# Performance work log

Measured on AMD Instinct MI355X. Metric: run time of the kernel, lower is better.

## Reference

```python
import jax, jax.numpy as jnp
import numpy as np
import math

D = 512
L = 1024
B = 2
N_SETS = 4
PLANES = 4
POS_PLANES = 16
TOTAL_PLANES = N_SETS * PLANES


def setup_inputs() -> dict:
    key = jax.random.key(0)
    ks = jax.random.split(key, 24)
    s = 0.02
    rn = lambda k, shp: jax.random.normal(k, shp, dtype=jnp.float32) * s
    inp = {
        "x": jax.random.normal(ks[0], (B, L, D), dtype=jnp.float32),
        # key encoder: Linear(D,D) -> GELU -> Linear(D,total_planes)
        "ke_w1": rn(ks[1], (D, D)), "ke_b1": jnp.zeros((D,), jnp.float32),
        "ke_w2": rn(ks[2], (D, TOTAL_PLANES)), "ke_b2": jnp.zeros((TOTAL_PLANES,), jnp.float32),
        # query encoder
        "qe_w1": rn(ks[3], (D, D)), "qe_b1": jnp.zeros((D,), jnp.float32),
        "qe_w2": rn(ks[4], (D, TOTAL_PLANES)), "qe_b2": jnp.zeros((TOTAL_PLANES,), jnp.float32),
        # to_value
        "v_w": rn(ks[5], (D, D)), "v_b": jnp.zeros((D,), jnp.float32),
        # to_out: LayerNorm(D) then Linear(D,D)
        "ln_g": jnp.ones((D,), jnp.float32), "ln_b": jnp.zeros((D,), jnp.float32),
        "out_w": rn(ks[6], (D, D)), "out_b": jnp.zeros((D,), jnp.float32),
        # set mixing weights, positional weight
        "set_weights": jnp.ones((N_SETS,), jnp.float32),
        "pos_weight": jnp.ones((1,), jnp.float32),
        # content_pos_gate: Linear(D, D//2) -> GELU -> Linear(D//2, 1) -> Sigmoid
        "gate_w1": rn(ks[7], (D, D // 2)), "gate_b1": jnp.zeros((D // 2,), jnp.float32),
        "gate_w2": rn(ks[8], (D // 2, 1)), "gate_b2": jnp.zeros((1,), jnp.float32),
        # positional frequencies (buffer)
        "pos_freqs": jnp.exp(jnp.arange(POS_PLANES, dtype=jnp.float32) * (-math.log(10000.0) / POS_PLANES)),
    }
    return inp


def reference(x, ke_w1, ke_b1, ke_w2, ke_b2, qe_w1, qe_b1, qe_w2, qe_b2,
              v_w, v_b, ln_g, ln_b, out_w, out_b, set_weights, pos_weight,
              gate_w1, gate_b1, gate_w2, gate_b2, pos_freqs):
    b, l, d = x.shape
    n_sets = set_weights.shape[0]
    total_planes = ke_w2.shape[1]
    planes = total_planes // n_sets

    gelu = lambda t: jax.nn.gelu(t, approximate=False)  # torch default GELU is exact

    key_phase = jnp.tanh(gelu(x @ ke_w1 + ke_b1) @ ke_w2 + ke_b2) * math.pi  # [B,L,P]
    query_phase = jnp.tanh(gelu(x @ qe_w1 + qe_b1) @ qe_w2 + qe_b2) * math.pi
    V = x @ v_w + v_b  # [B,L,D]

    kp = key_phase.reshape(b, l, n_sets, planes)
    qp = query_phase.reshape(b, l, n_sets, planes)
    w = jax.nn.softmax(set_weights)

    # complex phasor outer-product cumsum in real arithmetic:
    # bound = exp(i*kp) * V ; memory = cumsum_L(bound) ; retrieved = Re(memory * exp(-i*qp))
    Vb = V[:, :, None, None, :]                                   # [B,L,1,1,D]
    cum_re = jnp.cumsum(jnp.cos(kp)[..., None] * Vb, axis=1)      # [B,L,S,p,D]
    cum_im = jnp.cumsum(jnp.sin(kp)[..., None] * Vb, axis=1)
    retrieved = (cum_re * jnp.cos(qp)[..., None] + cum_im * jnp.sin(qp)[..., None]).sum(axis=3)  # [B,L,S,D]
    total_retrieved = jnp.einsum('blsd,s->bld', retrieved, w)

    # positional plane
    pos = jnp.arange(l, dtype=jnp.float32)[:, None]
    pos_phase = pos * pos_freqs * (2.0 * math.pi)                 # [L,PP]
    cp = jnp.cos(pos_phase)[None, :, :, None]                     # [1,L,PP,1]
    sp = jnp.sin(pos_phase)[None, :, :, None]
    Vp = V[:, :, None, :]                                          # [B,L,1,D]
    cumP_re = jnp.cumsum(cp * Vp, axis=1)                          # [B,L,PP,D]
    cumP_im = jnp.cumsum(sp * Vp, axis=1)
    retrieved_pos = (cumP_re * cp + cumP_im * sp).sum(axis=2)      # [B,L,D]

    gate = jax.nn.sigmoid(gelu(x @ gate_w1 + gate_b1) @ gate_w2 + gate_b2)  # [B,L,1]
    pos_contribution = jax.nn.sigmoid(pos_weight) * retrieved_pos
    total_retrieved = gate * total_retrieved + (1.0 - gate) * pos_contribution

    positions = jnp.arange(1, l + 1, dtype=jnp.float32)
    norm = jnp.sqrt(positions * planes)[None, :, None]
    h = total_retrieved / norm

    # to_out: LayerNorm then Linear
    mu = h.mean(axis=-1, keepdims=True)
    var = ((h - mu) ** 2).mean(axis=-1, keepdims=True)
    h_ln = (h - mu) / jnp.sqrt(var + 1e-5) * ln_g + ln_b
    return x + h_ln @ out_w + out_b
```

## Files before the change

kernel.cpp:

```cpp
#include <hip/hip_runtime.h>

typedef unsigned short u16;
typedef __attribute__((ext_vector_type(8))) __bf16 bf16x8;
typedef __attribute__((ext_vector_type(4))) float f32x4;

#define DI __device__ __forceinline__

DI u16 f2b(float f){ union{float f; unsigned u;} x; x.f = f; unsigned u = x.u;
  return (u16)((u + 0x7FFFu + ((u>>16)&1u)) >> 16); }

#define NCH 16
#define CLEN 64

__global__ __launch_bounds__(256) void k_prep(const float* __restrict__ x, u16* __restrict__ xb,
                            const float* w0, const float* w1, const float* w2, const float* w3, const float* w4,
                            u16* t0, u16* t1, u16* t2, u16* t3, u16* t4) {
  __shared__ u16 tile[32][33];
  int z = blockIdx.x;
  int t = threadIdx.x;
  if (z < 512) {
    int i = (z*256 + t)*8;
    float4 a = *(const float4*)(x+i);
    float4 b = *(const float4*)(x+i+4);
    unsigned o0 = (unsigned)f2b(a.x) | ((unsigned)f2b(a.y)<<16);
    unsigned o1 = (unsigned)f2b(a.z) | ((unsigned)f2b(a.w)<<16);
    unsigned o2 = (unsigned)f2b(b.x) | ((unsigned)f2b(b.y)<<16);
    unsigned o3 = (unsigned)f2b(b.z) | ((unsigned)f2b(b.w)<<16);
    *(uint4*)(xb+i) = make_uint4(o0,o1,o2,o3);
    return;
  }
  z -= 512;
  int which = z >> 8;
  int rem = z & 255;
  const float* src; u16* dst; int K, N;
  if (which==0){src=w0;dst=t0;K=512;N=512;}
  else if(which==1){src=w1;dst=t1;K=512;N=512;}
  else if(which==2){src=w2;dst=t2;K=512;N=512;}
  else if(which==3){src=w3;dst=t3;K=512;N=256;}
  else             {src=w4;dst=t4;K=512;N=512;}
  int n0 = (rem & 15)*32, k0 = (rem >> 4)*32;
  if (n0 >= N) return;
  int tx = t & 31, ty = t >> 5;
  #pragma unroll
  for (int r = 0; r < 4; r++) tile[ty + 8*r][tx] = f2b(src[(k0 + ty + 8*r)*N + n0 + tx]);
  __syncthreads();
  #pragma unroll
  for (int r = 0; r < 4; r++) dst[(n0 + ty + 8*r)*K + k0 + tx] = tile[tx][ty + 8*r];
}

#define GEMM64_LOOP(APTR, BPTR)                                                       \
  __shared__ short As[2][64][72];                                                     \
  __shared__ short Bs[2][64][72];                                                     \
  int t = threadIdx.x;                                                                \
  int lane = t & 63, wid = t >> 6;                                                    \
  int wm = (wid>>1)*32, wn = (wid&1)*32;                                              \
  int lr = lane & 15, ls = lane >> 4;                                                 \
  int srow = t >> 2, scol = (t & 3)*16;                                               \
  f32x4 acc[2][2];                                                                    \
  { f32x4 z_={0.f,0.f,0.f,0.f}; acc[0][0]=z_;acc[0][1]=z_;acc[1][0]=z_;acc[1][1]=z_; }\
  const u16* gA = (APTR) + (bm+srow)*512 + scol;                                      \
  const u16* gB = (BPTR) + (bn+srow)*512 + scol;                                      \
  bf16x8 rA0 = *(const bf16x8*)(gA);      bf16x8 rA1 = *(const bf16x8*)(gA+8);        \
// ... 10 lines not shown
    _Pragma("unroll")                                                                 \
    for (int ks = 0; ks < 2; ks++) {                                                  \
      _Pragma("unroll")                                                               \
      for (int mi = 0; mi < 2; mi++) {                                                \
        af_[mi][ks] = *(const bf16x8*)&As[cur][wm+mi*16+lr][ks*32+ls*8];              \
        bf_[mi][ks] = *(const bf16x8*)&Bs[cur][wn+mi*16+lr][ks*32+ls*8];              \
      }                                                                               \
    }                                                                                 \
    if (st < 7) {                                                                     \
      *(bf16x8*)&As[cur^1][srow][scol] = nA0; *(bf16x8*)&As[cur^1][srow][scol+8] = nA1; \
      *(bf16x8*)&Bs[cur^1][srow][scol] = nB0; *(bf16x8*)&Bs[cur^1][srow][scol+8] = nB1; \
    }                                                                                 \
    if (st < 6) {                                                                     \
      int kk = (st+2)*64;                                                             \
      nA0 = *(const bf16x8*)(gA+kk);    nA1 = *(const bf16x8*)(gA+kk+8);              \
      nB0 = *(const bf16x8*)(gB+kk);    nB1 = *(const bf16x8*)(gB+kk+8);              \
    }                                                                                 \
    _Pragma("unroll")                                                                 \
    for (int ks = 0; ks < 2; ks++)                                                    \
      _Pragma("unroll")                                                               \
      for (int mi = 0; mi < 2; mi++)                                                  \
        _Pragma("unroll")                                                             \
        for (int ni = 0; ni < 2; ni++)                                                \
          acc[mi][ni] = __builtin_amdgcn_mfma_f32_16x16x32_bf16(af_[mi][ks], bf_[ni][ks], acc[mi][ni], 0,0,0); \
    __syncthreads();                                                                  \
  }

__global__ __launch_bounds__(256) void k_gemm4(const u16* __restrict__ A, const u16* __restrict__ BTF,
                       const float* __restrict__ kb1, const float* __restrict__ qb1,
                       const float* __restrict__ vb,  const float* __restrict__ gbias1,
                       float* __restrict__ Hke, float* __restrict__ Hqe,
                       float* __restrict__ V,   float* __restrict__ Hg) {
  int bm = blockIdx.y*64, bn = blockIdx.x*64;
  GEMM64_LOOP(A, BTF)
  float* C; const float* bias; int nstr, nb; bool gel;
  if (bn < 512)       { C=Hke; bias=kb1;    nstr=512; nb=bn;      gel=true;  }
  else if (bn < 1024) { C=Hqe; bias=qb1;    nstr=512; nb=bn-512;  gel=true;  }
  else if (bn < 1536) { C=V;   bias=vb;     nstr=512; nb=bn-1024; gel=false; }
  else                { C=Hg;  bias=gbias1; nstr=256; nb=bn-1536; gel=true;  }
  #pragma unroll
  for (int mi = 0; mi < 2; mi++)
    #pragma unroll
    for (int ni = 0; ni < 2; ni++)
      #pragma unroll
      for (int r = 0; r < 4; r++) {
        int grow = bm + wm + mi*16 + ls*4 + r;
        int gcol = nb + wn + ni*16 + lr;
        float v = acc[mi][ni][r] + bias[gcol];
        if (gel) v = 0.5f*v*(1.0f + erff(v*0.70710678118654752f));
        C[grow*nstr + gcol] = v;
      }
}

__global__ __launch_bounds__(256) void k_gemm_out(const u16* __restrict__ A, const u16* __restrict__ BT,
                       const float* __restrict__ bias, const float* __restrict__ resid,
                       float* __restrict__ C) {
  int bm = blockIdx.y*64, bn = blockIdx.x*64;
  GEMM64_LOOP(A, BT)
  #pragma unroll
  for (int mi = 0; mi < 2; mi++)
    #pragma unroll
    for (int ni = 0; ni < 2; ni++)
      #pragma unroll
      for (int r = 0; r < 4; r++) {
        int grow = bm + wm + mi*16 + ls*4 + r;
        int gcol = bn + wn + ni*16 + lr;
        float v = acc[mi][ni][r] + bias[gcol] + resid[grow*512 + gcol];
        C[grow*512 + gcol] = v;
      }
}

__global__ __launch_bounds__(256) void k_phase(const float* __restrict__ Hke, const float* __restrict__ Hqe,
                        const float* __restrict__ Hg,
                        const float* __restrict__ kw2, const float* __restrict__ kb2,
                        const float* __restrict__ qw2, const float* __restrict__ qb2,
                        const float* __restrict__ gw2, const float* __restrict__ gb2,
                        const float* __restrict__ setw, const float* __restrict__ posw,
                        const float* __restrict__ freqs,
                        float* __restrict__ ub, float* __restrict__ ab) {
  int t = threadIdx.x;
  int wid = t >> 6, lane = t & 63;
  int r = blockIdx.x*4 + wid;
  int l = r & 1023;
  int p = lane & 15, s = lane >> 4;
  const float* hk = Hke + r*512 + s*128;
  const float* hq = Hqe + r*512 + s*128;
  float kps = 0.f, qps = 0.f;
  for (int i0 = 0; i0 < 128; i0 += 4) {
    float4 hkv = *(const float4*)(hk + i0);
    float4 hqv = *(const float4*)(hq + i0);
    int kb = (s*128 + i0)*16 + p;
    kps += hkv.x * kw2[kb];      qps += hqv.x * qw2[kb];
    kps += hkv.y * kw2[kb+16];   qps += hqv.y * qw2[kb+16];
    kps += hkv.z * kw2[kb+32];   qps += hqv.z * qw2[kb+32];
    kps += hkv.w * kw2[kb+48];   qps += hqv.w * qw2[kb+48];
  }
  kps += __shfl_xor(kps, 16); kps += __shfl_xor(kps, 32);
  qps += __shfl_xor(qps, 16); qps += __shfl_xor(qps, 32);
  const float PI = 3.14159265358979323846f;
  float kph = tanhf(kps + kb2[p]) * PI;
  float qph = tanhf(qps + qb2[p]) * PI;
  const float* hg = Hg + r*256;
  float4 hgv = *(const float4*)(hg + lane*4);
  float gp = hgv.x*gw2[lane*4] + hgv.y*gw2[lane*4+1]
           + hgv.z*gw2[lane*4+2] + hgv.w*gw2[lane*4+3];
  #pragma unroll
  for (int m = 1; m <= 32; m <<= 1) gp += __shfl_xor(gp, m);
  float gate = 1.f/(1.f + expf(-(gp + gb2[0])));
  float pph = (float)l * freqs[p] * 6.2831853071795864769f;
  float s0=setw[0], s1=setw[1], s2=setw[2], s3=setw[3];
  float mx = fmaxf(fmaxf(s0,s1), fmaxf(s2,s3));
  float e0=expf(s0-mx), e1=expf(s1-mx), e2=expf(s2-mx), e3=expf(s3-mx);
  float esum = e0+e1+e2+e3;
  int si = p >> 2;
  float wsel = (si==0? e0 : si==1? e1 : si==2? e2 : e3) / esum;
  float sigpw = 1.f/(1.f + expf(-posw[0]));
  float invnorm = rsqrtf((float)(l+1) * 4.0f);
  if (lane < 16) {
    float sk, ck, sq, cq, sp, cp;
    sincosf(kph, &sk, &ck);
    sincosf(qph, &sq, &cq);
    sincosf(pph, &sp, &cp);
    float* urow = ub + r*64;
    float* arow = ab + r*64;
    urow[p]      = ck;
    urow[16 + p] = sk;
    urow[32 + p] = cp;
    urow[48 + p] = sp;
    float ga = gate * wsel * invnorm;
    float pa = (1.f - gate) * sigpw * invnorm;
    arow[p]      = ga * cq;
    arow[16 + p] = ga * sq;
    arow[32 + p] = pa * cp;
    arow[48 + p] = pa * sp;
  }
}

__global__ __launch_bounds__(256) void k_scanA(const float* __restrict__ ub, const float* __restrict__ V,
                        float* __restrict__ P) {
  __shared__ float ul[CLEN][64];
  __shared__ float vl[CLEN][64];
  int t = threadIdx.x;
  int d0 = blockIdx.x*64; int c = blockIdx.y; int b = blockIdx.z;
  int srow = t >> 2, scol = (t & 3)*16;
  {
    const float* up = ub + (b*1024 + c*CLEN + srow)*64 + scol;
    *(float4*)&ul[srow][scol]    = *(const float4*)up;
    *(float4*)&ul[srow][scol+4]  = *(const float4*)(up+4);
    *(float4*)&ul[srow][scol+8]  = *(const float4*)(up+8);
    *(float4*)&ul[srow][scol+12] = *(const float4*)(up+12);
    const float* vp = V + (b*1024 + c*CLEN + srow)*512 + d0 + scol;
    *(float4*)&vl[srow][scol]    = *(const float4*)vp;
    *(float4*)&vl[srow][scol+4]  = *(const float4*)(vp+4);
    *(float4*)&vl[srow][scol+8]  = *(const float4*)(vp+8);
    *(float4*)&vl[srow][scol+12] = *(const float4*)(vp+12);
  }
  __syncthreads();
  int dd = t & 63, kg = t >> 6;
  float acc[16];
  #pragma unroll
  for (int i=0;i<16;i++) acc[i]=0.f;
  for (int tt = 0; tt < CLEN; tt++) {
    float vv = vl[tt][dd];
    #pragma unroll
    for (int i=0;i<16;i++) acc[i] += ul[tt][kg*16+i]*vv;
  }
  float* pp = P + (((b*NCH + c)*64) + kg*16)*512 + d0 + dd;
  #pragma unroll
  for (int i=0;i<16;i++) pp[i*512] = acc[i];
}

__global__ __launch_bounds__(256) void k_scanB(float* __restrict__ P) {
  int tid = blockIdx.x*256 + threadIdx.x;
  int b = tid >> 15;
  int k = (tid >> 9) & 63;
  int d = tid & 511;
  float run = 0.f;
  float* base = P + ((b*NCH)*64 + k)*512 + d;
  for (int c = 0; c < NCH; c++) {
    float v = base[c*64*512];
    base[c*64*512] = run;
    run += v;
  }
}

__global__ __launch_bounds__(256) void k_scanC(const float* __restrict__ ub, const float* __restrict__ ab,
                        const float* __restrict__ V, const float* __restrict__ P,
                        float* __restrict__ h) {
  __shared__ float ul[CLEN][64];
  __shared__ float al[CLEN][64];
  int t = threadIdx.x;
  int c = blockIdx.y; int b = blockIdx.z;
  int srow = t >> 2, scol = (t & 3)*16;
  {
    const float* up = ub + (b*1024 + c*CLEN + srow)*64 + scol;
    *(float4*)&ul[srow][scol]    = *(const float4*)up;
    *(float4*)&ul[srow][scol+4]  = *(const float4*)(up+4);
    *(float4*)&ul[srow][scol+8]  = *(const float4*)(up+8);
    *(float4*)&ul[srow][scol+12] = *(const float4*)(up+12);
    const float* ap = ab + (b*1024 + c*CLEN + srow)*64 + scol;
    *(float4*)&al[srow][scol]    = *(const float4*)ap;
    *(float4*)&al[srow][scol+4]  = *(const float4*)(ap+4);
    *(float4*)&al[srow][scol+8]  = *(const float4*)(ap+8);
    *(float4*)&al[srow][scol+12] = *(const float4*)(ap+12);
  }
  __syncthreads();
  int kg = t & 3;
  int di = t >> 2;
  int d = blockIdx.x*64 + di;
  float s[16];
  const float* pb = P + ((b*NCH + c)*64 + kg*16)*512 + d;
  #pragma unroll
  for (int k = 0; k < 16; k++) s[k] = pb[k*512];
  const float* vrow = V + (b*1024 + c*CLEN)*512 + d;
  float* hrow = h + (b*1024 + c*CLEN)*512 + d;
  const float4* ul4 = (const float4*)&ul[0][0];
  const float4* al4 = (const float4*)&al[0][0];
  for (int tt = 0; tt < CLEN; tt++) {
    float vv = vrow[tt*512];
    float4 u0 = ul4[tt*16 + kg*4 + 0];
    float4 u1 = ul4[tt*16 + kg*4 + 1];
    float4 u2 = ul4[tt*16 + kg*4 + 2];
    float4 u3 = ul4[tt*16 + kg*4 + 3];
    float4 a0 = al4[tt*16 + kg*4 + 0];
    float4 a1 = al4[tt*16 + kg*4 + 1];
    float4 a2 = al4[tt*16 + kg*4 + 2];
    float4 a3 = al4[tt*16 + kg*4 + 3];
    float h0=0.f, h1=0.f, h2=0.f, h3=0.f;
    s[0]  += u0.x*vv; h0 += a0.x*s[0];
    s[1]  += u0.y*vv; h1 += a0.y*s[1];
    s[2]  += u0.z*vv; h2 += a0.z*s[2];
    s[3]  += u0.w*vv; h3 += a0.w*s[3];
    s[4]  += u1.x*vv; h0 += a1.x*s[4];
    s[5]  += u1.y*vv; h1 += a1.y*s[5];
    s[6]  += u1.z*vv; h2 += a1.z*s[6];
    s[7]  += u1.w*vv; h3 += a1.w*s[7];
    s[8]  += u2.x*vv; h0 += a2.x*s[8];
    s[9]  += u2.y*vv; h1 += a2.y*s[9];
    s[10] += u2.z*vv; h2 += a2.z*s[10];
    s[11] += u2.w*vv; h3 += a2.w*s[11];
    s[12] += u3.x*vv; h0 += a3.x*s[12];
    s[13] += u3.y*vv; h1 += a3.y*s[13];
    s[14] += u3.z*vv; h2 += a3.z*s[14];
    s[15] += u3.w*vv; h3 += a3.w*s[15];
    float hp = (h0+h1)+(h2+h3);
    hp += __shfl_xor(hp, 1);
    hp += __shfl_xor(hp, 2);
    if (kg == 0) hrow[tt*512] = hp;
  }
}

__global__ __launch_bounds__(256) void k_ln(const float* __restrict__ h, const float* __restrict__ g,
                     const float* __restrict__ bta, u16* __restrict__ hln) {
  int t = threadIdx.x;
  int wid = t >> 6, lane = t & 63;
  int r = blockIdx.x*4 + wid;
  const float* hr = h + r*512;
  float4 v0 = *(const float4*)(hr + lane*8);
  float4 v1 = *(const float4*)(hr + lane*8 + 4);
  float vals[8] = {v0.x,v0.y,v0.z,v0.w,v1.x,v1.y,v1.z,v1.w};
  float sum = 0.f, sq = 0.f;
  #pragma unroll
  for (int i=0;i<8;i++){ sum += vals[i]; sq += vals[i]*vals[i]; }
  #pragma unroll
  for (int m = 1; m <= 32; m <<= 1){ sum += __shfl_xor(sum, m); sq += __shfl_xor(sq, m); }
  float mu = sum * (1.f/512.f);
  float var = sq * (1.f/512.f) - mu*mu;
  float rstd = rsqrtf(var + 1e-5f);
  unsigned o[4];
  #pragma unroll
  for (int i=0;i<4;i++){
    u16 lo = f2b((vals[2*i]  -mu)*rstd*g[lane*8+2*i]   + bta[lane*8+2*i]);
    u16 hi = f2b((vals[2*i+1]-mu)*rstd*g[lane*8+2*i+1] + bta[lane*8+2*i+1]);
    o[i] = (unsigned)lo | ((unsigned)hi << 16);
  }
  uint4 ov = make_uint4(o[0],o[1],o[2],o[3]);
  *(uint4*)(hln + r*512 + lane*8) = ov;
}

extern "C" void kernel_launch(void* const* d_in, const int* in_sizes, int n_in,
                              void* d_out, int out_size, void* d_ws, size_t ws_size,
                              hipStream_t stream) {
  const float* x       = (const float*)d_in[0];
  const float* ke_w1   = (const float*)d_in[1];
  const float* ke_b1   = (const float*)d_in[2];
  const float* ke_w2   = (const float*)d_in[3];
  const float* ke_b2   = (const float*)d_in[4];
  const float* qe_w1   = (const float*)d_in[5];
  const float* qe_b1   = (const float*)d_in[6];
  const float* qe_w2   = (const float*)d_in[7];
  const float* qe_b2   = (const float*)d_in[8];
  const float* v_w     = (const float*)d_in[9];
  const float* v_b     = (const float*)d_in[10];
  const float* ln_g    = (const float*)d_in[11];
  const float* ln_b    = (const float*)d_in[12];
  const float* out_w   = (const float*)d_in[13];
  const float* out_b   = (const float*)d_in[14];
  const float* setw    = (const float*)d_in[15];
  const float* posw    = (const float*)d_in[16];
  const float* gate_w1 = (const float*)d_in[17];
  const float* gate_b1 = (const float*)d_in[18];
  const float* gate_w2 = (const float*)d_in[19];
  const float* gate_b2 = (const float*)d_in[20];
  const float* freqs   = (const float*)d_in[21];
  float* out = (float*)d_out;

  char* ws = (char*)d_ws;
  u16*   xb  = (u16*)(ws + 0);
  u16*   BTF = (u16*)(ws + 2097152);
  u16*   oT  = (u16*)(ws + 3932160);
  float* Hke = (float*)(ws + 4456448);
  float* Hqe = (float*)(ws + 8650752);
  float* Hg  = (float*)(ws + 12845056);
  float* V   = (float*)(ws + 14942208);
  float* ubf = (float*)(ws + 19136512);
  float* abf = (float*)(ws + 19660800);
  float* P   = (float*)(ws + 20185088);
  float* h   = Hke;
  u16*   hln = (u16*)Hqe;

  u16* keT = BTF;
  u16* qeT = BTF + 512*512;
  u16* vT  = BTF + 1024*512;
  u16* gT  = BTF + 1536*512;

  k_prep<<<512 + 5*256, 256, 0, stream>>>(x, xb, ke_w1,qe_w1,v_w,gate_w1,out_w,
                                          keT,qeT,vT,gT,oT);
  k_gemm4<<<dim3(28,32),256,0,stream>>>(xb, BTF, ke_b1, qe_b1, v_b, gate_b1,
                                        Hke, Hqe, V, Hg);
  k_phase<<<512,256,0,stream>>>(Hke,Hqe,Hg, ke_w2,ke_b2, qe_w2,qe_b2,
                                gate_w2,gate_b2, setw,posw,freqs, ubf,abf);
  k_scanA<<<dim3(8,NCH,2),256,0,stream>>>(ubf, V, P);
  k_scanB<<<256,256,0,stream>>>(P);
  k_scanC<<<dim3(8,NCH,2),256,0,stream>>>(ubf, abf, V, P, h);
  k_ln<<<512,256,0,stream>>>(h, ln_g, ln_b, hln);
  k_gemm_out<<<dim3(8,32),256,0,stream>>>(hln, oT, out_b, x, out);
}
```

Before: 78.64 us.

## Fuse LayerNorm into output GEMM and scanB into scanA via last-block counter

Removes the standalone LayerNorm kernel: the output GEMM now computes per-row mean and rstd from fp32 h, then normalizes and converts to bf16 while staging A tiles into double-buffered LDS. Folds the cross-chunk prefix pass into scanA, where the last arriving block per (batch, d-tile) runs the carry scan, detected with an atomic counter that k_phase resets. This saves two launches and the hln round trip. The cost is that each GEMM block re-reads its 64 rows of h to get statistics, and the tail scan runs serially in only 16 blocks.

```diff
diff --git a/kernel.cpp b/kernel.cpp
--- a/kernel.cpp
+++ b/kernel.cpp
@@ -8,6 +8,12 @@
 
 DI u16 f2b(float f){ union{float f; unsigned u;} x; x.f = f; unsigned u = x.u;
   return (u16)((u + 0x7FFFu + ((u>>16)&1u)) >> 16); }
+
+DI uint2 ln4(float4 a, float4 g, float4 c, float mu, float rs) {
+  unsigned lo = (unsigned)f2b((a.x-mu)*rs*g.x+c.x) | ((unsigned)f2b((a.y-mu)*rs*g.y+c.y)<<16);
+  unsigned hi = (unsigned)f2b((a.z-mu)*rs*g.z+c.z) | ((unsigned)f2b((a.w-mu)*rs*g.w+c.w)<<16);
+  return make_uint2(lo,hi);
+}
 
 #define NCH 16
 #define CLEN 64
@@ -124,11 +130,104 @@
       }
 }
 
-__global__ __launch_bounds__(256) void k_gemm_out(const u16* __restrict__ A, const u16* __restrict__ BT,
+__global__ __launch_bounds__(256) void k_gemm_out_ln(
+                       const float* __restrict__ h,   const float* __restrict__ lng,
+                       const float* __restrict__ lnb, const u16* __restrict__ BT,
                        const float* __restrict__ bias, const float* __restrict__ resid,
                        float* __restrict__ C) {
+  __shared__ short As[2][64][72];
+  __shared__ short Bs[2][64][72];
+  __shared__ float mu_s[64], rs_s[64];
+  int t = threadIdx.x;
   int bm = blockIdx.y*64, bn = blockIdx.x*64;
-  GEMM64_LOOP(A, BT)
+  int lane = t & 63, wid = t >> 6;
+  int wm = (wid>>1)*32, wn = (wid&1)*32;
+  int lr = lane & 15, ls = lane >> 4;
+  int srow = t >> 2, scol = (t & 3)*16;
+  {
+    int rr = t >> 2, q = t & 3;
+    const float* hr = h + (bm + rr)*512 + q*128;
+    float sum = 0.f, sq = 0.f;
+    #pragma unroll
+    for (int i = 0; i < 128; i += 4) {
+      float4 v = *(const float4*)(hr + i);
+      sum += (v.x+v.y)+(v.z+v.w);
+      sq  += (v.x*v.x+v.y*v.y)+(v.z*v.z+v.w*v.w);
+    }
+    sum += __shfl_xor(sum,1); sum += __shfl_xor(sum,2);
+    sq  += __shfl_xor(sq,1);  sq  += __shfl_xor(sq,2);
+    if (q == 0) {
+      float m_ = sum * (1.f/512.f);
+      float var = sq * (1.f/512.f) - m_*m_;
+      mu_s[rr] = m_;
+      rs_s[rr] = rsqrtf(var + 1e-5f);
+    }
+  }
+  __syncthreads();
+  const float mu = mu_s[srow], rs = rs_s[srow];
+  f32x4 acc[2][2];
+  { f32x4 z_={0.f,0.f,0.f,0.f}; acc[0][0]=z_;acc[0][1]=z_;acc[1][0]=z_;acc[1][1]=z_; }
+  const float* gA = h + (bm+srow)*512 + scol;
+  const u16*  gB = BT + (bn+srow)*512 + scol;
+  float4 a0,a1,a2,a3, n0,n1,n2,n3;
+  bf16x8 rB0, rB1, nB0, nB1;
+  a0=*(const float4*)(gA);    a1=*(const float4*)(gA+4);
+  a2=*(const float4*)(gA+8);  a3=*(const float4*)(gA+12);
+  rB0=*(const bf16x8*)(gB);   rB1=*(const bf16x8*)(gB+8);
+  n0=*(const float4*)(gA+64); n1=*(const float4*)(gA+68);
+  n2=*(const float4*)(gA+72); n3=*(const float4*)(gA+76);
+  nB0=*(const bf16x8*)(gB+64); nB1=*(const bf16x8*)(gB+72);
+  {
+    float4 g0=*(const float4*)(lng+scol),   g1=*(const float4*)(lng+scol+4);
+    float4 g2=*(const float4*)(lng+scol+8), g3=*(const float4*)(lng+scol+12);
+    float4 c0=*(const float4*)(lnb+scol),   c1=*(const float4*)(lnb+scol+4);
+    float4 c2=*(const float4*)(lnb+scol+8), c3=*(const float4*)(lnb+scol+12);
+    uint2 p0=ln4(a0,g0,c0,mu,rs), p1=ln4(a1,g1,c1,mu,rs);
+    uint2 p2=ln4(a2,g2,c2,mu,rs), p3=ln4(a3,g3,c3,mu,rs);
+    *(uint4*)&As[0][srow][scol]   = make_uint4(p0.x,p0.y,p1.x,p1.y);
+    *(uint4*)&As[0][srow][scol+8] = make_uint4(p2.x,p2.y,p3.x,p3.y);
+    *(bf16x8*)&Bs[0][srow][scol] = rB0; *(bf16x8*)&Bs[0][srow][scol+8] = rB1;
+  }
+  __syncthreads();
+  #pragma unroll
+  for (int st = 0; st < 8; st++) {
+    int cur = st & 1;
+    bf16x8 af_[2][2], bf_[2][2];
+    #pragma unroll
+    for (int ks = 0; ks < 2; ks++) {
+      #pragma unroll
+      for (int mi = 0; mi < 2; mi++) {
+        af_[mi][ks] = *(const bf16x8*)&As[cur][wm+mi*16+lr][ks*32+ls*8];
+        bf_[mi][ks] = *(const bf16x8*)&Bs[cur][wn+mi*16+lr][ks*32+ls*8];
+      }
+    }
+    if (st < 7) {
+      int kc = (st+1)*64 + scol;
+      float4 g0=*(const float4*)(lng+kc),   g1=*(const float4*)(lng+kc+4);
+      float4 g2=*(const float4*)(lng+kc+8), g3=*(const float4*)(lng+kc+12);
+      float4 c0=*(const float4*)(lnb+kc),   c1=*(const float4*)(lnb+kc+4);
+      float4 c2=*(const float4*)(lnb+kc+8), c3=*(const float4*)(lnb+kc+12);
+      uint2 p0=ln4(n0,g0,c0,mu,rs), p1=ln4(n1,g1,c1,mu,rs);
+      uint2 p2=ln4(n2,g2,c2,mu,rs), p3=ln4(n3,g3,c3,mu,rs);
+      *(uint4*)&As[cur^1][srow][scol]   = make_uint4(p0.x,p0.y,p1.x,p1.y);
+      *(uint4*)&As[cur^1][srow][scol+8] = make_uint4(p2.x,p2.y,p3.x,p3.y);
+      *(bf16x8*)&Bs[cur^1][srow][scol] = nB0; *(bf16x8*)&Bs[cur^1][srow][scol+8] = nB1;
+    }
+    if (st < 6) {
+      int kk = (st+2)*64;
+      n0=*(const float4*)(gA+kk);    n1=*(const float4*)(gA+kk+4);
+      n2=*(const float4*)(gA+kk+8);  n3=*(const float4*)(gA+kk+12);
+      nB0=*(const bf16x8*)(gB+kk);   nB1=*(const bf16x8*)(gB+kk+8);
+    }
+    #pragma unroll
+    for (int ks = 0; ks < 2; ks++)
+      #pragma unroll
+      for (int mi = 0; mi < 2; mi++)
+        #pragma unroll
+        for (int ni = 0; ni < 2; ni++)
+          acc[mi][ni] = __builtin_amdgcn_mfma_f32_16x16x32_bf16(af_[mi][ks], bf_[ni][ks], acc[mi][ni], 0,0,0);
+    __syncthreads();
+  }
   #pragma unroll
   for (int mi = 0; mi < 2; mi++)
     #pragma unroll
@@ -149,8 +248,10 @@
                         const float* __restrict__ gw2, const float* __restrict__ gb2,
                         const float* __restrict__ setw, const float* __restrict__ posw,
                         const float* __restrict__ freqs,
-                        float* __restrict__ ub, float* __restrict__ ab) {
+                        float* __restrict__ ub, float* __restrict__ ab,
+                        int* __restrict__ counters) {
   int t = threadIdx.x;
+  if (blockIdx.x == 0 && t < 16) counters[t] = 0;
   int wid = t >> 6, lane = t & 63;
   int r = blockIdx.x*4 + wid;
   int l = r & 1023;
@@ -209,9 +310,10 @@
 }
 
 __global__ __launch_bounds__(256) void k_scanA(const float* __restrict__ ub, const float* __restrict__ V,
-                        float* __restrict__ P) {
+                        float* __restrict__ P, int* __restrict__ counters) {
   __shared__ float ul[CLEN][64];
   __shared__ float vl[CLEN][64];
+  __shared__ int lastf;
   int t = threadIdx.x;
   int d0 = blockIdx.x*64; int c = blockIdx.y; int b = blockIdx.z;
   int srow = t >> 2, scol = (t & 3)*16;
@@ -240,19 +342,26 @@
   float* pp = P + (((b*NCH + c)*64) + kg*16)*512 + d0 + dd;
   #pragma unroll
   for (int i=0;i<16;i++) pp[i*512] = acc[i];
-}
-
-__global__ __launch_bounds__(256) void k_scanB(float* __restrict__ P) {
-  int tid = blockIdx.x*256 + threadIdx.x;
-  int b = tid >> 15;
-  int k = (tid >> 9) & 63;
-  int d = tid & 511;
-  float run = 0.f;
-  float* base = P + ((b*NCH)*64 + k)*512 + d;
-  for (int c = 0; c < NCH; c++) {
-    float v = base[c*64*512];
-    base[c*64*512] = run;
-    run += v;
+  __threadfence();
+  if (t == 0) {
+    int old = atomicAdd(&counters[b*8 + blockIdx.x], 1);
+    lastf = (old == NCH-1) ? 1 : 0;
+  }
+  __syncthreads();
+  if (lastf) {
+    int d = d0 + (t & 63);
+    int kq0 = (t >> 6) * 16;
+    #pragma unroll 1
+    for (int kq = 0; kq < 16; kq++) {
+      float run = 0.f;
+      float* base = P + ((b*NCH)*64 + kq0 + kq)*512 + d;
+      #pragma unroll 1
+      for (int c2 = 0; c2 < NCH; c2++) {
+        float v = base[c2*64*512];
+        base[c2*64*512] = run;
+        run += v;
+      }
+    }
   }
 }
 
@@ -322,34 +431,6 @@
   }
 }
 
-__global__ __launch_bounds__(256) void k_ln(const float* __restrict__ h, const float* __restrict__ g,
-                     const float* __restrict__ bta, u16* __restrict__ hln) {
-  int t = threadIdx.x;
-  int wid = t >> 6, lane = t & 63;
-  int r = blockIdx.x*4 + wid;
-  const float* hr = h + r*512;
-  float4 v0 = *(const float4*)(hr + lane*8);
-  float4 v1 = *(const float4*)(hr + lane*8 + 4);
-  float vals[8] = {v0.x,v0.y,v0.z,v0.w,v1.x,v1.y,v1.z,v1.w};
-  float sum = 0.f, sq = 0.f;
-  #pragma unroll
-  for (int i=0;i<8;i++){ sum += vals[i]; sq += vals[i]*vals[i]; }
-  #pragma unroll
-  for (int m = 1; m <= 32; m <<= 1){ sum += __shfl_xor(sum, m); sq += __shfl_xor(sq, m); }
-  float mu = sum * (1.f/512.f);
-  float var = sq * (1.f/512.f) - mu*mu;
-  float rstd = rsqrtf(var + 1e-5f);
-  unsigned o[4];
-  #pragma unroll
-  for (int i=0;i<4;i++){
-    u16 lo = f2b((vals[2*i]  -mu)*rstd*g[lane*8+2*i]   + bta[lane*8+2*i]);
-    u16 hi = f2b((vals[2*i+1]-mu)*rstd*g[lane*8+2*i+1] + bta[lane*8+2*i+1]);
-    o[i] = (unsigned)lo | ((unsigned)hi << 16);
-  }
-  uint4 ov = make_uint4(o[0],o[1],o[2],o[3]);
-  *(uint4*)(hln + r*512 + lane*8) = ov;
-}
-
 extern "C" void kernel_launch(void* const* d_in, const int* in_sizes, int n_in,
                               void* d_out, int out_size, void* d_ws, size_t ws_size,
                               hipStream_t stream) {
@@ -389,7 +470,7 @@
   float* abf = (float*)(ws + 19660800);
   float* P   = (float*)(ws + 20185088);
   float* h   = Hke;
-  u16*   hln = (u16*)Hqe;
+  int* counters = (int*)ws;
 
   u16* keT = BTF;
   u16* qeT = BTF + 512*512;
@@ -401,10 +482,8 @@
   k_gemm4<<<dim3(28,32),256,0,stream>>>(xb, BTF, ke_b1, qe_b1, v_b, gate_b1,
                                         Hke, Hqe, V, Hg);
   k_phase<<<512,256,0,stream>>>(Hke,Hqe,Hg, ke_w2,ke_b2, qe_w2,qe_b2,
-                                gate_w2,gate_b2, setw,posw,freqs, ubf,abf);
-  k_scanA<<<dim3(8,NCH,2),256,0,stream>>>(ubf, V, P);
-  k_scanB<<<256,256,0,stream>>>(P);
+                                gate_w2,gate_b2, setw,posw,freqs, ubf,abf, counters);
+  k_scanA<<<dim3(8,NCH,2),256,0,stream>>>(ubf, V, P, counters);
   k_scanC<<<dim3(8,NCH,2),256,0,stream>>>(ubf, abf, V, P, h);
-  k_ln<<<512,256,0,stream>>>(h, ln_g, ln_b, hln);
-  k_gemm_out<<<dim3(8,32),256,0,stream>>>(hln, oT, out_b, x, out);
-}
+  k_gemm_out_ln<<<dim3(8,32),256,0,stream>>>(h, ln_g, ln_b, oT, out_b, x, out);
+}
```

New measurement: 172.7 us. 120% more time.

## Fuse chunked scan kernels into one with last-block carry and spin wait

Applied to the files above, without the earlier changes.

Merges the three scan kernels (chunk sums, carry prefix, chunk replay) into one kernel. Blocks of the same batch/column group count arrivals with an atomic counter. The last arriving block computes the exclusive prefix over chunks, then releases a flag that the other blocks spin on. The replay phase now reads V from the shared-memory tile already loaded instead of from global memory, and the counters are reset inside k_phase. This removes two launches and a re-read of V. The cost is inter-block spin-waiting, which relies on all 256 blocks being co-resident, and a serial carry pass done by one block per group.

```diff
diff --git a/kernel.cpp b/kernel.cpp
--- a/kernel.cpp
+++ b/kernel.cpp
@@ -149,8 +149,10 @@
                         const float* __restrict__ gw2, const float* __restrict__ gb2,
                         const float* __restrict__ setw, const float* __restrict__ posw,
                         const float* __restrict__ freqs,
-                        float* __restrict__ ub, float* __restrict__ ab) {
+                        float* __restrict__ ub, float* __restrict__ ab,
+                        int* __restrict__ gate) {
   int t = threadIdx.x;
+  if (blockIdx.x == 0 && t < 32) gate[t] = 0;
   int wid = t >> 6, lane = t & 63;
   int r = blockIdx.x*4 + wid;
   int l = r & 1023;
@@ -178,7 +180,7 @@
            + hgv.z*gw2[lane*4+2] + hgv.w*gw2[lane*4+3];
   #pragma unroll
   for (int m = 1; m <= 32; m <<= 1) gp += __shfl_xor(gp, m);
-  float gate = 1.f/(1.f + expf(-(gp + gb2[0])));
+  float gate_v = 1.f/(1.f + expf(-(gp + gb2[0])));
   float pph = (float)l * freqs[p] * 6.2831853071795864769f;
   float s0=setw[0], s1=setw[1], s2=setw[2], s3=setw[3];
   float mx = fmaxf(fmaxf(s0,s1), fmaxf(s2,s3));
@@ -199,8 +201,8 @@
     urow[16 + p] = sk;
     urow[32 + p] = cp;
     urow[48 + p] = sp;
-    float ga = gate * wsel * invnorm;
-    float pa = (1.f - gate) * sigpw * invnorm;
+    float ga = gate_v * wsel * invnorm;
+    float pa = (1.f - gate_v) * sigpw * invnorm;
     arow[p]      = ga * cq;
     arow[16 + p] = ga * sq;
     arow[32 + p] = pa * cp;
@@ -208,12 +210,16 @@
   }
 }
 
-__global__ __launch_bounds__(256) void k_scanA(const float* __restrict__ ub, const float* __restrict__ V,
-                        float* __restrict__ P) {
+__global__ __launch_bounds__(256) void k_scan(const float* __restrict__ ub, const float* __restrict__ ab,
+                        const float* __restrict__ V, float* __restrict__ P,
+                        float* __restrict__ h, int* __restrict__ gate) {
   __shared__ float ul[CLEN][64];
   __shared__ float vl[CLEN][64];
+  __shared__ float al[CLEN][64];
+  __shared__ int amlast;
   int t = threadIdx.x;
   int d0 = blockIdx.x*64; int c = blockIdx.y; int b = blockIdx.z;
+  int g = b*8 + blockIdx.x;
   int srow = t >> 2, scol = (t & 3)*16;
   {
     const float* up = ub + (b*1024 + c*CLEN + srow)*64 + scol;
@@ -226,50 +232,6 @@
     *(float4*)&vl[srow][scol+4]  = *(const float4*)(vp+4);
     *(float4*)&vl[srow][scol+8]  = *(const float4*)(vp+8);
     *(float4*)&vl[srow][scol+12] = *(const float4*)(vp+12);
-  }
-  __syncthreads();
-  int dd = t & 63, kg = t >> 6;
-  float acc[16];
-  #pragma unroll
-  for (int i=0;i<16;i++) acc[i]=0.f;
-  for (int tt = 0; tt < CLEN; tt++) {
-    float vv = vl[tt][dd];
-    #pragma unroll
-    for (int i=0;i<16;i++) acc[i] += ul[tt][kg*16+i]*vv;
-  }
-  float* pp = P + (((b*NCH + c)*64) + kg*16)*512 + d0 + dd;
-  #pragma unroll
-  for (int i=0;i<16;i++) pp[i*512] = acc[i];
-}
-
-__global__ __launch_bounds__(256) void k_scanB(float* __restrict__ P) {
-  int tid = blockIdx.x*256 + threadIdx.x;
-  int b = tid >> 15;
-  int k = (tid >> 9) & 63;
-  int d = tid & 511;
-  float run = 0.f;
-  float* base = P + ((b*NCH)*64 + k)*512 + d;
-  for (int c = 0; c < NCH; c++) {
-    float v = base[c*64*512];
-    base[c*64*512] = run;
-    run += v;
-  }
-}
-
-__global__ __launch_bounds__(256) void k_scanC(const float* __restrict__ ub, const float* __restrict__ ab,
-                        const float* __restrict__ V, const float* __restrict__ P,
-                        float* __restrict__ h) {
-  __shared__ float ul[CLEN][64];
-  __shared__ float al[CLEN][64];
-  int t = threadIdx.x;
-  int c = blockIdx.y; int b = blockIdx.z;
-  int srow = t >> 2, scol = (t & 3)*16;
-  {
-    const float* up = ub + (b*1024 + c*CLEN + srow)*64 + scol;
-    *(float4*)&ul[srow][scol]    = *(const float4*)up;
-    *(float4*)&ul[srow][scol+4]  = *(const float4*)(up+4);
-    *(float4*)&ul[srow][scol+8]  = *(const float4*)(up+8);
-    *(float4*)&ul[srow][scol+12] = *(const float4*)(up+12);
     const float* ap = ab + (b*1024 + c*CLEN + srow)*64 + scol;
     *(float4*)&al[srow][scol]    = *(const float4*)ap;
     *(float4*)&al[srow][scol+4]  = *(const float4*)(ap+4);
@@ -277,19 +239,61 @@
     *(float4*)&al[srow][scol+12] = *(const float4*)(ap+12);
   }
   __syncthreads();
+  {
+    int dd = t & 63, kg = t >> 6;
+    float acc[16];
+    #pragma unroll
+    for (int i=0;i<16;i++) acc[i]=0.f;
+    for (int tt = 0; tt < CLEN; tt++) {
+      float vv = vl[tt][dd];
+      #pragma unroll
+      for (int i=0;i<16;i++) acc[i] += ul[tt][kg*16+i]*vv;
+    }
+    float* pp = P + (((b*NCH + c)*64) + kg*16)*512 + d0 + dd;
+    #pragma unroll
+    for (int i=0;i<16;i++) pp[i*512] = acc[i];
+  }
+  __threadfence();
+  __syncthreads();
+  if (t == 0) amlast = (atomicAdd(&gate[g], 1) == NCH-1) ? 1 : 0;
+  __syncthreads();
+  if (amlast) {
+    int d = d0 + (t & 63);
+    int k0 = (t >> 6) * 16;
+    float run[16];
+    #pragma unroll
+    for (int i=0;i<16;i++) run[i]=0.f;
+    for (int cc = 0; cc < NCH; cc++) {
+      float* base = P + ((b*NCH + cc)*64 + k0)*512 + d;
+      float v[16];
+      #pragma unroll
+      for (int i=0;i<16;i++) v[i] = base[i*512];
+      #pragma unroll
+      for (int i=0;i<16;i++) { base[i*512] = run[i]; run[i] += v[i]; }
+    }
+    __threadfence();
+    __syncthreads();
+    if (t == 0)
+      __hip_atomic_store(&gate[16+g], 1, __ATOMIC_RELEASE, __HIP_MEMORY_SCOPE_AGENT);
+  }
+  if (t == 0) {
+    while (__hip_atomic_load(&gate[16+g], __ATOMIC_ACQUIRE, __HIP_MEMORY_SCOPE_AGENT) == 0)
+      __builtin_amdgcn_s_sleep(8);
+  }
+  __syncthreads();
+  __threadfence();
   int kg = t & 3;
   int di = t >> 2;
-  int d = blockIdx.x*64 + di;
+  int d = d0 + di;
   float s[16];
   const float* pb = P + ((b*NCH + c)*64 + kg*16)*512 + d;
   #pragma unroll
   for (int k = 0; k < 16; k++) s[k] = pb[k*512];
-  const float* vrow = V + (b*1024 + c*CLEN)*512 + d;
   float* hrow = h + (b*1024 + c*CLEN)*512 + d;
   const float4* ul4 = (const float4*)&ul[0][0];
   const float4* al4 = (const float4*)&al[0][0];
   for (int tt = 0; tt < CLEN; tt++) {
-    float vv = vrow[tt*512];
+    float vv = vl[tt][di];
     float4 u0 = ul4[tt*16 + kg*4 + 0];
     float4 u1 = ul4[tt*16 + kg*4 + 1];
     float4 u2 = ul4[tt*16 + kg*4 + 2];
@@ -388,6 +392,7 @@
   float* ubf = (float*)(ws + 19136512);
   float* abf = (float*)(ws + 19660800);
   float* P   = (float*)(ws + 20185088);
+  int*   gate = (int*)(ws + 24379392);
   float* h   = Hke;
   u16*   hln = (u16*)Hqe;
 
@@ -401,10 +406,8 @@
   k_gemm4<<<dim3(28,32),256,0,stream>>>(xb, BTF, ke_b1, qe_b1, v_b, gate_b1,
                                         Hke, Hqe, V, Hg);
   k_phase<<<512,256,0,stream>>>(Hke,Hqe,Hg, ke_w2,ke_b2, qe_w2,qe_b2,
-                                gate_w2,gate_b2, setw,posw,freqs, ubf,abf);
-  k_scanA<<<dim3(8,NCH,2),256,0,stream>>>(ubf, V, P);
-  k_scanB<<<256,256,0,stream>>>(P);
-  k_scanC<<<dim3(8,NCH,2),256,0,stream>>>(ubf, abf, V, P, h);
+                                gate_w2,gate_b2, setw,posw,freqs, ubf,abf, gate);
+  k_scan<<<dim3(8,NCH,2),256,0,stream>>>(ubf, abf, V, P, h, gate);
   k_ln<<<512,256,0,stream>>>(h, ln_g, ln_b, hln);
   k_gemm_out<<<dim3(8,32),256,0,stream>>>(hln, oT, out_b, x, out);
 }
```

Result: slower. 181.1 us (+130.3%).

## Fuse phase, chunked scan and layernorm into one cooperative kernel

Applied to the files above, without the earlier changes.

Replaces the five separate launches (phase, scanA, scanB, scanC, layernorm) with a single cooperative kernel of 256 blocks, using grid-wide syncs between the stages. The V tile loaded into shared memory for the chunk-sum stage is reused in the final scan stage instead of being re-read from global memory. The aim is to cut kernel launch gaps and some global traffic. In exchange it adds four grid barriers with thread fences, and each block now does twice the per-row work in the phase and layernorm stages.

```diff
diff --git a/kernel.cpp b/kernel.cpp
--- a/kernel.cpp
+++ b/kernel.cpp
@@ -1,4 +1,7 @@
 #include <hip/hip_runtime.h>
+#include <hip/hip_cooperative_groups.h>
+
+namespace cg = cooperative_groups;
 
 typedef unsigned short u16;
 typedef __attribute__((ext_vector_type(8))) __bf16 bf16x8;
@@ -142,79 +145,89 @@
       }
 }
 
-__global__ __launch_bounds__(256) void k_phase(const float* __restrict__ Hke, const float* __restrict__ Hqe,
-                        const float* __restrict__ Hg,
-                        const float* __restrict__ kw2, const float* __restrict__ kb2,
-                        const float* __restrict__ qw2, const float* __restrict__ qb2,
-                        const float* __restrict__ gw2, const float* __restrict__ gb2,
-                        const float* __restrict__ setw, const float* __restrict__ posw,
-                        const float* __restrict__ freqs,
-                        float* __restrict__ ub, float* __restrict__ ab) {
-  int t = threadIdx.x;
-  int wid = t >> 6, lane = t & 63;
-  int r = blockIdx.x*4 + wid;
-  int l = r & 1023;
-  int p = lane & 15, s = lane >> 4;
-  const float* hk = Hke + r*512 + s*128;
-  const float* hq = Hqe + r*512 + s*128;
-  float kps = 0.f, qps = 0.f;
-  for (int i0 = 0; i0 < 128; i0 += 4) {
-    float4 hkv = *(const float4*)(hk + i0);
-    float4 hqv = *(const float4*)(hq + i0);
-    int kb = (s*128 + i0)*16 + p;
-    kps += hkv.x * kw2[kb];      qps += hqv.x * qw2[kb];
-    kps += hkv.y * kw2[kb+16];   qps += hqv.y * qw2[kb+16];
-    kps += hkv.z * kw2[kb+32];   qps += hqv.z * qw2[kb+32];
-    kps += hkv.w * kw2[kb+48];   qps += hqv.w * qw2[kb+48];
-  }
-  kps += __shfl_xor(kps, 16); kps += __shfl_xor(kps, 32);
-  qps += __shfl_xor(qps, 16); qps += __shfl_xor(qps, 32);
-  const float PI = 3.14159265358979323846f;
-  float kph = tanhf(kps + kb2[p]) * PI;
-  float qph = tanhf(qps + qb2[p]) * PI;
-  const float* hg = Hg + r*256;
-  float4 hgv = *(const float4*)(hg + lane*4);
-  float gp = hgv.x*gw2[lane*4] + hgv.y*gw2[lane*4+1]
-           + hgv.z*gw2[lane*4+2] + hgv.w*gw2[lane*4+3];
-  #pragma unroll
-  for (int m = 1; m <= 32; m <<= 1) gp += __shfl_xor(gp, m);
-  float gate = 1.f/(1.f + expf(-(gp + gb2[0])));
-  float pph = (float)l * freqs[p] * 6.2831853071795864769f;
-  float s0=setw[0], s1=setw[1], s2=setw[2], s3=setw[3];
-  float mx = fmaxf(fmaxf(s0,s1), fmaxf(s2,s3));
-  float e0=expf(s0-mx), e1=expf(s1-mx), e2=expf(s2-mx), e3=expf(s3-mx);
-  float esum = e0+e1+e2+e3;
-  int si = p >> 2;
-  float wsel = (si==0? e0 : si==1? e1 : si==2? e2 : e3) / esum;
-  float sigpw = 1.f/(1.f + expf(-posw[0]));
-  float invnorm = rsqrtf((float)(l+1) * 4.0f);
-  if (lane < 16) {
-    float sk, ck, sq, cq, sp, cp;
-    sincosf(kph, &sk, &ck);
-    sincosf(qph, &sq, &cq);
-    sincosf(pph, &sp, &cp);
-    float* urow = ub + r*64;
-    float* arow = ab + r*64;
-    urow[p]      = ck;
-    urow[16 + p] = sk;
-    urow[32 + p] = cp;
-    urow[48 + p] = sp;
-    float ga = gate * wsel * invnorm;
-    float pa = (1.f - gate) * sigpw * invnorm;
-    arow[p]      = ga * cq;
-    arow[16 + p] = ga * sq;
-    arow[32 + p] = pa * cp;
-    arow[48 + p] = pa * sp;
-  }
-}
-
-__global__ __launch_bounds__(256) void k_scanA(const float* __restrict__ ub, const float* __restrict__ V,
-                        float* __restrict__ P) {
+__global__ __launch_bounds__(256) void k_mid(
+    const float* __restrict__ Hke, const float* __restrict__ Hqe, const float* __restrict__ Hg,
+    const float* __restrict__ kw2, const float* __restrict__ kb2,
+    const float* __restrict__ qw2, const float* __restrict__ qb2,
+    const float* __restrict__ gw2, const float* __restrict__ gb2,
+    const float* __restrict__ setw, const float* __restrict__ posw,
+    const float* __restrict__ freqs,
+    float* __restrict__ ub, float* __restrict__ ab,
+    const float* __restrict__ V, float* __restrict__ P,
+    float* __restrict__ h,
+    const float* __restrict__ lng, const float* __restrict__ lnb,
+    u16* __restrict__ hln) {
   __shared__ float ul[CLEN][64];
   __shared__ float vl[CLEN][64];
+  __shared__ float al[CLEN][64];
+  cg::grid_group grid = cg::this_grid();
   int t = threadIdx.x;
-  int d0 = blockIdx.x*64; int c = blockIdx.y; int b = blockIdx.z;
+  int bid = blockIdx.x;
+  int wid = t >> 6, lane = t & 63;
+
+  for (int rr = 0; rr < 2; rr++) {
+    int r = bid*8 + rr*4 + wid;
+    int l = r & 1023;
+    int p = lane & 15, s = lane >> 4;
+    const float* hk = Hke + r*512 + s*128;
+    const float* hq = Hqe + r*512 + s*128;
+    float kps = 0.f, qps = 0.f;
+    for (int i0 = 0; i0 < 128; i0 += 4) {
+      float4 hkv = *(const float4*)(hk + i0);
+      float4 hqv = *(const float4*)(hq + i0);
+      int kb = (s*128 + i0)*16 + p;
+      kps += hkv.x * kw2[kb];      qps += hqv.x * qw2[kb];
+      kps += hkv.y * kw2[kb+16];   qps += hqv.y * qw2[kb+16];
+      kps += hkv.z * kw2[kb+32];   qps += hqv.z * qw2[kb+32];
+      kps += hkv.w * kw2[kb+48];   qps += hqv.w * qw2[kb+48];
+    }
+    kps += __shfl_xor(kps, 16); kps += __shfl_xor(kps, 32);
+    qps += __shfl_xor(qps, 16); qps += __shfl_xor(qps, 32);
+    const float PI = 3.14159265358979323846f;
+    float kph = tanhf(kps + kb2[p]) * PI;
+    float qph = tanhf(qps + qb2[p]) * PI;
+    const float* hg = Hg + r*256;
+    float4 hgv = *(const float4*)(hg + lane*4);
+    float gp = hgv.x*gw2[lane*4] + hgv.y*gw2[lane*4+1]
+             + hgv.z*gw2[lane*4+2] + hgv.w*gw2[lane*4+3];
+    #pragma unroll
+    for (int m = 1; m <= 32; m <<= 1) gp += __shfl_xor(gp, m);
+    float gate = 1.f/(1.f + expf(-(gp + gb2[0])));
+    float pph = (float)l * freqs[p] * 6.2831853071795864769f;
+    float s0=setw[0], s1=setw[1], s2=setw[2], s3=setw[3];
+    float mx = fmaxf(fmaxf(s0,s1), fmaxf(s2,s3));
+    float e0=expf(s0-mx), e1=expf(s1-mx), e2=expf(s2-mx), e3=expf(s3-mx);
+    float esum = e0+e1+e2+e3;
+    int si = p >> 2;
+    float wsel = (si==0? e0 : si==1? e1 : si==2? e2 : e3) / esum;
+    float sigpw = 1.f/(1.f + expf(-posw[0]));
+    float invnorm = rsqrtf((float)(l+1) * 4.0f);
+    if (lane < 16) {
+      float sk, ck, sq, cq, sp, cp;
+      sincosf(kph, &sk, &ck);
+      sincosf(qph, &sq, &cq);
+      sincosf(pph, &sp, &cp);
+      float* urow = ub + r*64;
+      float* arow = ab + r*64;
+      urow[p]      = ck;
+      urow[16 + p] = sk;
+      urow[32 + p] = cp;
+      urow[48 + p] = sp;
+      float ga = gate * wsel * invnorm;
+      float pa = (1.f - gate) * sigpw * invnorm;
+      arow[p]      = ga * cq;
+      arow[16 + p] = ga * sq;
+      arow[32 + p] = pa * cp;
+      arow[48 + p] = pa * sp;
+    }
+  }
+  __threadfence();
+  grid.sync();
+
+  int dblk = bid & 7, c = (bid >> 3) & 15, b = bid >> 7;
+  int d0 = dblk*64;
   int srow = t >> 2, scol = (t & 3)*16;
+
   {
     const float* up = ub + (b*1024 + c*CLEN + srow)*64 + scol;
     *(float4*)&ul[srow][scol]    = *(const float4*)up;
@@ -226,128 +239,115 @@
     *(float4*)&vl[srow][scol+4]  = *(const float4*)(vp+4);
     *(float4*)&vl[srow][scol+8]  = *(const float4*)(vp+8);
     *(float4*)&vl[srow][scol+12] = *(const float4*)(vp+12);
-  }
-  __syncthreads();
-  int dd = t & 63, kg = t >> 6;
-  float acc[16];
-  #pragma unroll
-  for (int i=0;i<16;i++) acc[i]=0.f;
-  for (int tt = 0; tt < CLEN; tt++) {
-    float vv = vl[tt][dd];
-    #pragma unroll
-    for (int i=0;i<16;i++) acc[i] += ul[tt][kg*16+i]*vv;
-  }
-  float* pp = P + (((b*NCH + c)*64) + kg*16)*512 + d0 + dd;
-  #pragma unroll
-  for (int i=0;i<16;i++) pp[i*512] = acc[i];
-}
-
-__global__ __launch_bounds__(256) void k_scanB(float* __restrict__ P) {
-  int tid = blockIdx.x*256 + threadIdx.x;
-  int b = tid >> 15;
-  int k = (tid >> 9) & 63;
-  int d = tid & 511;
-  float run = 0.f;
-  float* base = P + ((b*NCH)*64 + k)*512 + d;
-  for (int c = 0; c < NCH; c++) {
-    float v = base[c*64*512];
-    base[c*64*512] = run;
-    run += v;
-  }
-}
-
-__global__ __launch_bounds__(256) void k_scanC(const float* __restrict__ ub, const float* __restrict__ ab,
-                        const float* __restrict__ V, const float* __restrict__ P,
-                        float* __restrict__ h) {
-  __shared__ float ul[CLEN][64];
-  __shared__ float al[CLEN][64];
-  int t = threadIdx.x;
-  int c = blockIdx.y; int b = blockIdx.z;
-  int srow = t >> 2, scol = (t & 3)*16;
-  {
-    const float* up = ub + (b*1024 + c*CLEN + srow)*64 + scol;
-    *(float4*)&ul[srow][scol]    = *(const float4*)up;
-    *(float4*)&ul[srow][scol+4]  = *(const float4*)(up+4);
-    *(float4*)&ul[srow][scol+8]  = *(const float4*)(up+8);
-    *(float4*)&ul[srow][scol+12] = *(const float4*)(up+12);
     const float* ap = ab + (b*1024 + c*CLEN + srow)*64 + scol;
     *(float4*)&al[srow][scol]    = *(const float4*)ap;
     *(float4*)&al[srow][scol+4]  = *(const float4*)(ap+4);
     *(float4*)&al[srow][scol+8]  = *(const float4*)(ap+8);
     *(float4*)&al[srow][scol+12] = *(const float4*)(ap+12);
-  }
-  __syncthreads();
-  int kg = t & 3;
-  int di = t >> 2;
-  int d = blockIdx.x*64 + di;
-  float s[16];
-  const float* pb = P + ((b*NCH + c)*64 + kg*16)*512 + d;
-  #pragma unroll
-  for (int k = 0; k < 16; k++) s[k] = pb[k*512];
-  const float* vrow = V + (b*1024 + c*CLEN)*512 + d;
-  float* hrow = h + (b*1024 + c*CLEN)*512 + d;
-  const float4* ul4 = (const float4*)&ul[0][0];
-  const float4* al4 = (const float4*)&al[0][0];
-  for (int tt = 0; tt < CLEN; tt++) {
-    float vv = vrow[tt*512];
-    float4 u0 = ul4[tt*16 + kg*4 + 0];
-    float4 u1 = ul4[tt*16 + kg*4 + 1];
-    float4 u2 = ul4[tt*16 + kg*4 + 2];
-    float4 u3 = ul4[tt*16 + kg*4 + 3];
-    float4 a0 = al4[tt*16 + kg*4 + 0];
-    float4 a1 = al4[tt*16 + kg*4 + 1];
-    float4 a2 = al4[tt*16 + kg*4 + 2];
-    float4 a3 = al4[tt*16 + kg*4 + 3];
-    float h0=0.f, h1=0.f, h2=0.f, h3=0.f;
-    s[0]  += u0.x*vv; h0 += a0.x*s[0];
-    s[1]  += u0.y*vv; h1 += a0.y*s[1];
-    s[2]  += u0.z*vv; h2 += a0.z*s[2];
-    s[3]  += u0.w*vv; h3 += a0.w*s[3];
-    s[4]  += u1.x*vv; h0 += a1.x*s[4];
-    s[5]  += u1.y*vv; h1 += a1.y*s[5];
-    s[6]  += u1.z*vv; h2 += a1.z*s[6];
-    s[7]  += u1.w*vv; h3 += a1.w*s[7];
-    s[8]  += u2.x*vv; h0 += a2.x*s[8];
-    s[9]  += u2.y*vv; h1 += a2.y*s[9];
-    s[10] += u2.z*vv; h2 += a2.z*s[10];
-    s[11] += u2.w*vv; h3 += a2.w*s[11];
-    s[12] += u3.x*vv; h0 += a3.x*s[12];
-    s[13] += u3.y*vv; h1 += a3.y*s[13];
-    s[14] += u3.z*vv; h2 += a3.z*s[14];
-    s[15] += u3.w*vv; h3 += a3.w*s[15];
-    float hp = (h0+h1)+(h2+h3);
-    hp += __shfl_xor(hp, 1);
-    hp += __shfl_xor(hp, 2);
-    if (kg == 0) hrow[tt*512] = hp;
-  }
-}
-
-__global__ __launch_bounds__(256) void k_ln(const float* __restrict__ h, const float* __restrict__ g,
-                     const float* __restrict__ bta, u16* __restrict__ hln) {
-  int t = threadIdx.x;
-  int wid = t >> 6, lane = t & 63;
-  int r = blockIdx.x*4 + wid;
-  const float* hr = h + r*512;
-  float4 v0 = *(const float4*)(hr + lane*8);
-  float4 v1 = *(const float4*)(hr + lane*8 + 4);
-  float vals[8] = {v0.x,v0.y,v0.z,v0.w,v1.x,v1.y,v1.z,v1.w};
-  float sum = 0.f, sq = 0.f;
-  #pragma unroll
-  for (int i=0;i<8;i++){ sum += vals[i]; sq += vals[i]*vals[i]; }
-  #pragma unroll
-  for (int m = 1; m <= 32; m <<= 1){ sum += __shfl_xor(sum, m); sq += __shfl_xor(sq, m); }
-  float mu = sum * (1.f/512.f);
-  float var = sq * (1.f/512.f) - mu*mu;
-  float rstd = rsqrtf(var + 1e-5f);
-  unsigned o[4];
-  #pragma unroll
-  for (int i=0;i<4;i++){
-    u16 lo = f2b((vals[2*i]  -mu)*rstd*g[lane*8+2*i]   + bta[lane*8+2*i]);
-    u16 hi = f2b((vals[2*i+1]-mu)*rstd*g[lane*8+2*i+1] + bta[lane*8+2*i+1]);
-    o[i] = (unsigned)lo | ((unsigned)hi << 16);
-  }
-  uint4 ov = make_uint4(o[0],o[1],o[2],o[3]);
-  *(uint4*)(hln + r*512 + lane*8) = ov;
+    __syncthreads();
+    int dd = t & 63, kg = t >> 6;
+    float acc[16];
+    #pragma unroll
+    for (int i=0;i<16;i++) acc[i]=0.f;
+    for (int tt = 0; tt < CLEN; tt++) {
+      float vv = vl[tt][dd];
+      #pragma unroll
+      for (int i=0;i<16;i++) acc[i] += ul[tt][kg*16+i]*vv;
+    }
+    float* pp = P + (((b*NCH + c)*64) + kg*16)*512 + d0 + dd;
+    #pragma unroll
+    for (int i=0;i<16;i++) pp[i*512] = acc[i];
+  }
+  __threadfence();
+  grid.sync();
+
+  {
+    int tid = bid*256 + t;
+    int bb = tid >> 15;
+    int k = (tid >> 9) & 63;
+    int d = tid & 511;
+    float run = 0.f;
+    float* base = P + ((bb*NCH)*64 + k)*512 + d;
+    for (int cc = 0; cc < NCH; cc++) {
+      float v = base[cc*64*512];
+      base[cc*64*512] = run;
+      run += v;
+    }
+  }
+  __threadfence();
+  grid.sync();
+
+  {
+    int kg = t & 3;
+    int di = t >> 2;
+    int d = d0 + di;
+    float s[16];
+    const float* pb = P + ((b*NCH + c)*64 + kg*16)*512 + d;
+    #pragma unroll
+    for (int k = 0; k < 16; k++) s[k] = pb[k*512];
+    float* hrow = h + (b*1024 + c*CLEN)*512 + d;
+    const float4* ul4 = (const float4*)&ul[0][0];
+    const float4* al4 = (const float4*)&al[0][0];
+    for (int tt = 0; tt < CLEN; tt++) {
+      float vv = vl[tt][di];
+      float4 u0 = ul4[tt*16 + kg*4 + 0];
+      float4 u1 = ul4[tt*16 + kg*4 + 1];
+      float4 u2 = ul4[tt*16 + kg*4 + 2];
+      float4 u3 = ul4[tt*16 + kg*4 + 3];
+      float4 a0 = al4[tt*16 + kg*4 + 0];
+      float4 a1 = al4[tt*16 + kg*4 + 1];
+      float4 a2 = al4[tt*16 + kg*4 + 2];
+      float4 a3 = al4[tt*16 + kg*4 + 3];
+      float h0=0.f, h1=0.f, h2=0.f, h3=0.f;
+      s[0]  += u0.x*vv; h0 += a0.x*s[0];
+      s[1]  += u0.y*vv; h1 += a0.y*s[1];
+      s[2]  += u0.z*vv; h2 += a0.z*s[2];
+      s[3]  += u0.w*vv; h3 += a0.w*s[3];
+      s[4]  += u1.x*vv; h0 += a1.x*s[4];
+      s[5]  += u1.y*vv; h1 += a1.y*s[5];
+      s[6]  += u1.z*vv; h2 += a1.z*s[6];
+      s[7]  += u1.w*vv; h3 += a1.w*s[7];
+      s[8]  += u2.x*vv; h0 += a2.x*s[8];
+      s[9]  += u2.y*vv; h1 += a2.y*s[9];
+      s[10] += u2.z*vv; h2 += a2.z*s[10];
+      s[11] += u2.w*vv; h3 += a2.w*s[11];
+      s[12] += u3.x*vv; h0 += a3.x*s[12];
+      s[13] += u3.y*vv; h1 += a3.y*s[13];
+      s[14] += u3.z*vv; h2 += a3.z*s[14];
+      s[15] += u3.w*vv; h3 += a3.w*s[15];
+      float hp = (h0+h1)+(h2+h3);
+      hp += __shfl_xor(hp, 1);
+      hp += __shfl_xor(hp, 2);
+      if (kg == 0) hrow[tt*512] = hp;
+    }
+  }
+  __threadfence();
+  grid.sync();
+
+  for (int rr = 0; rr < 2; rr++) {
+    int r = bid*8 + rr*4 + wid;
+    const float* hr = h + r*512;
+    float4 v0 = *(const float4*)(hr + lane*8);
+    float4 v1 = *(const float4*)(hr + lane*8 + 4);
+    float vals[8] = {v0.x,v0.y,v0.z,v0.w,v1.x,v1.y,v1.z,v1.w};
+    float sum = 0.f, sq = 0.f;
+    #pragma unroll
+    for (int i=0;i<8;i++){ sum += vals[i]; sq += vals[i]*vals[i]; }
+    #pragma unroll
+    for (int m = 1; m <= 32; m <<= 1){ sum += __shfl_xor(sum, m); sq += __shfl_xor(sq, m); }
+    float mu = sum * (1.f/512.f);
+    float var = sq * (1.f/512.f) - mu*mu;
+    float rstd = rsqrtf(var + 1e-5f);
+    unsigned o[4];
+    #pragma unroll
+    for (int i=0;i<4;i++){
+      u16 lo = f2b((vals[2*i]  -mu)*rstd*lng[lane*8+2*i]   + lnb[lane*8+2*i]);
+      u16 hi = f2b((vals[2*i+1]-mu)*rstd*lng[lane*8+2*i+1] + lnb[lane*8+2*i+1]);
+      o[i] = (unsigned)lo | ((unsigned)hi << 16);
+    }
+    uint4 ov = make_uint4(o[0],o[1],o[2],o[3]);
+    *(uint4*)(hln + r*512 + lane*8) = ov;
+  }
 }
 
 extern "C" void kernel_launch(void* const* d_in, const int* in_sizes, int n_in,
@@ -400,11 +400,16 @@
                                           keT,qeT,vT,gT,oT);
   k_gemm4<<<dim3(28,32),256,0,stream>>>(xb, BTF, ke_b1, qe_b1, v_b, gate_b1,
                                         Hke, Hqe, V, Hg);
-  k_phase<<<512,256,0,stream>>>(Hke,Hqe,Hg, ke_w2,ke_b2, qe_w2,qe_b2,
-                                gate_w2,gate_b2, setw,posw,freqs, ubf,abf);
-  k_scanA<<<dim3(8,NCH,2),256,0,stream>>>(ubf, V, P);
-  k_scanB<<<256,256,0,stream>>>(P);
-  k_scanC<<<dim3(8,NCH,2),256,0,stream>>>(ubf, abf, V, P, h);
-  k_ln<<<512,256,0,stream>>>(h, ln_g, ln_b, hln);
+  {
+    void* kargs[] = {
+      (void*)&Hke, (void*)&Hqe, (void*)&Hg,
+      (void*)&ke_w2, (void*)&ke_b2, (void*)&qe_w2, (void*)&qe_b2,
+      (void*)&gate_w2, (void*)&gate_b2, (void*)&setw, (void*)&posw,
+      (void*)&freqs, (void*)&ubf, (void*)&abf,
+      (void*)&V, (void*)&P, (void*)&h,
+      (void*)&ln_g, (void*)&ln_b, (void*)&hln
+    };
+    hipLaunchCooperativeKernel((void*)k_mid, dim3(256), dim3(256), kargs, 0, stream);
+  }
   k_gemm_out<<<dim3(8,32),256,0,stream>>>(hln, oT, out_b, x, out);
 }
```

Measured after the change: 280.6 us. +256.8%, slower.
